# Performance work log

Hardware: AMD Instinct MI355X
Metric: run time of the kernel (lower is better)

The kernel has to match this reference:

```python
import jax, jax.numpy as jnp
import numpy as np

B, P, C = 32, 8732, 21
TOP_K = 200
CONF_THRESH = 0.01
NMS_THRESH = 0.45
VAR0, VAR1 = 0.1, 0.2  # VOC PRIOR_BOX VARIANCE


def setup_inputs() -> dict:
    key = jax.random.key(0)
    k1, k2, k3 = jax.random.split(key, 3)
    loc_data = jax.random.normal(k1, (B, P, 4), jnp.float32)
    conf_data = jax.random.uniform(k2, (B, P, C), jnp.float32)
    prior_data = jax.random.uniform(k3, (P, 4), jnp.float32)
    return {"loc_data": loc_data, "conf_data": conf_data, "prior_data": prior_data}


def _decode(loc, priors):
    # priors are (cx, cy, w, h); returns (x1, y1, x2, y2)
    cxcy = priors[:, :2] + loc[:, :2] * VAR0 * priors[:, 2:]
    wh = priors[:, 2:] * jnp.exp(loc[:, 2:] * VAR1)
    x1y1 = cxcy - wh * 0.5
    return jnp.concatenate([x1y1, x1y1 + wh], axis=1)  # [P,4]


def _nms_class(boxes, scores):
    # boxes [P,4], scores [P] -> [TOP_K,5] rows of (score, x1, y1, x2, y2)
    s = jnp.where(scores > CONF_THRESH, scores, -1.0)
    top_s, idx = jax.lax.top_k(s, TOP_K)          # descending scores
    b = boxes[idx]                                 # [K,4]
    valid = top_s > CONF_THRESH
    x1, y1, x2, y2 = b[:, 0], b[:, 1], b[:, 2], b[:, 3]
    area = (x2 - x1) * (y2 - y1)
    # pairwise intersection / IoU [K,K]
    xx1 = jnp.maximum(x1[:, None], x1[None, :])
    yy1 = jnp.maximum(y1[:, None], y1[None, :])
    xx2 = jnp.minimum(x2[:, None], x2[None, :])
    yy2 = jnp.minimum(y2[:, None], y2[None, :])
    inter = jnp.clip(xx2 - xx1, 0.0) * jnp.clip(yy2 - yy1, 0.0)
    union = area[:, None] + area[None, :] - inter
    iou = inter / union
    ar = jnp.arange(TOP_K)

    def step(carry, j):
        kept, suppressed = carry
        is_kept = valid[j] & ~suppressed[j]
        kept = kept.at[j].set(is_kept)
        suppressed = suppressed | (is_kept & (iou[j] > NMS_THRESH) & (ar > j))
        return (kept, suppressed), None

    (kept, _), _ = jax.lax.scan(
        step, (jnp.zeros(TOP_K, bool), jnp.zeros(TOP_K, bool)), ar)
    # compact kept rows to the front (matches output[i, cl, :count] = ...)
    pos = jnp.cumsum(kept) - 1
    safe = jnp.where(kept, pos, TOP_K)
    rows = jnp.concatenate([top_s[:, None], b], axis=1)  # [K,5]
    out = jnp.zeros((TOP_K + 1, 5), rows.dtype).at[safe].set(rows)[:TOP_K]
    return out


def reference(loc_data, conf_data, prior_data):
    def per_image(loc, conf):
        boxes = _decode(loc, prior_data)           # [P,4]
        return jax.vmap(lambda s: _nms_class(boxes, s), in_axes=1)(conf)  # [C,K,5]

    out = jax.vmap(per_image)(loc_data, conf_data)  # [B,C,K,5]
    return out.at[:, 0].set(0.0)  # class 0 (background) is skipped in original
```

## Files before the change

### kernel.cpp

```cpp
#include <hip/hip_runtime.h>
#include <stdint.h>

#define B_ 32
#define P_ 8732
#define C_ 21
#define TOPK 200
#define TGT 228
#define TGT0 300
#define SUBCAP 28
#define NCH2 35
#define NSLOT (NCH2 * SUBCAP)
#define CONF_T 0.01f
#define NMS_T 0.45f
#define NT 512
#define KV4 5
#define NTASK (B_ * C_)

__device__ __forceinline__ uint32_t f2s(float f) {
    uint32_t u = __float_as_uint(f);
    return (u & 0x80000000u) ? ~u : (u | 0x80000000u);
}
__device__ __forceinline__ float s2f(uint32_t s) {
    uint32_t b = (s & 0x80000000u) ? (s & 0x7FFFFFFFu) : ~s;
    return __uint_as_float(b);
}
__device__ __forceinline__ uint32_t keyof(float v) {
    return f2s((v > CONF_T) ? v : -1.0f);
}
__device__ __forceinline__ uint32_t thr0() {
    return f2s(1.0f - (float)TGT0 / (float)P_);
}

__global__ __launch_bounds__(256) void scatter_cands(const float* __restrict__ conf,
                                                     uint32_t* __restrict__ gccnt,
                                                     uint64_t* __restrict__ gcand) {
    const int b = blockIdx.x / NCH2;
    const int ch = blockIdx.x % NCH2;
    const int p0 = ch * 256;
    const int n = min(256, P_ - p0);
    const int tid = threadIdx.x;
    const int lane = tid & 63;
    const int cs = tid >> 6;
    __shared__ float tile[256 * C_];
    const float4* src4 = (const float4*)(conf + ((size_t)b * P_ + p0) * C_);
    float4* tile4 = (float4*)tile;
    const int tot4 = (n * C_) >> 2;
    for (int i = tid; i < tot4; i += 256) tile4[i] = src4[i];
    __syncthreads();
    const uint32_t T0 = thr0();
    for (int c = (cs == 0 ? 4 : cs); c < C_; c += 4) {
        uint32_t kk[4];
        #pragma unroll
        for (int k = 0; k < 4; ++k) {
            const int r = lane + 64 * k;
            if (r < n) kk[k] = keyof(tile[r * C_ + c]);
            else       kk[k] = 0u;
        }
        const unsigned long long m0 = __ballot(kk[0] >= T0);
        const unsigned long long m1 = __ballot(kk[1] >= T0);
        const unsigned long long m2 = __ballot(kk[2] >= T0);
        const unsigned long long m3 = __ballot(kk[3] >= T0);
        const int c0 = __popcll(m0), c1 = __popcll(m1), c2 = __popcll(m2), c3 = __popcll(m3);
        const int total = c0 + c1 + c2 + c3;
        const int task = b * C_ + c;
        uint64_t* dst = gcand + ((size_t)task * NCH2 + ch) * SUBCAP;
        {
            const unsigned long long below = (1ull << lane) - 1ull;
            const int cum[4] = {0, c0, c0 + c1, c0 + c1 + c2};
            const unsigned long long mm[4] = {m0, m1, m2, m3};
            #pragma unroll
            for (int k = 0; k < 4; ++k) {
                if (kk[k] >= T0) {
                    const int pos = cum[k] + __popcll(mm[k] & below);
                    if (pos < SUBCAP) {
                        const int p = p0 + lane + 64 * k;
                        dst[pos] = ((uint64_t)kk[k] << 32) | (uint32_t)(~(uint32_t)p);
                    }
                }
            }
        }
        if (lane == 0) gccnt[(size_t)task * NCH2 + ch] = (uint32_t)total;
    }
}

template<bool HASWS>
__global__ __launch_bounds__(NT, 6) void detect_kernel(
    const float* __restrict__ loc, const float* __restrict__ prior,
    const uint32_t* __restrict__ gccnt, const uint64_t* __restrict__ gcand,
    const float* __restrict__ conf, float* __restrict__ out)
{
    const int task = blockIdx.x;
    const int b = task / C_;
    const int c = task % C_;
    const int tid = threadIdx.x;
    const int lane = tid & 63;
    float* outp = out + (size_t)task * TOPK * 5;

    if (c == 0) {
        for (int e = tid; e < TOPK * 5; e += NT) outp[e] = 0.0f;
        return;
    }

    __shared__ uint64_t cand[256];
    __shared__ float4 bbox[TOPK];
    __shared__ float bs[TOPK];
    __shared__ float sar[TOPK];
    __shared__ unsigned long long msk[TOPK * 4];
    __shared__ unsigned long long vmask[4];
    __shared__ int order[TOPK];
    __shared__ int s_cnt, s_nk;
    __shared__ int s_c2[2];
    __shared__ int s_c3[3];
    __shared__ uint32_t s_ccnt[NCH2];
    __shared__ int s_gc, s_bad;

    const uint32_t T0 = thr0();

    if (tid == 0) s_cnt = 0;
    if (tid < 2) s_c2[tid] = 0;
    if (tid < 3) s_c3[tid] = 0;
    if (HASWS && tid < NCH2) s_ccnt[tid] = gccnt[(size_t)task * NCH2 + tid];
    for (int i2 = tid; i2 < TOPK * 4; i2 += NT) msk[i2] = 0ull;
    __syncthreads();
    if (HASWS && tid < 64) {
        uint32_t cc = (lane < NCH2) ? s_ccnt[lane] : 0u;
        int bad = (cc > SUBCAP) ? 1 : 0;
        int tot = (int)cc;
        #pragma unroll
        for (int d = 1; d < 64; d <<= 1) {
            tot += __shfl_down(tot, d);
            bad |= __shfl_down(bad, d);
        }
        if (lane == 0) { s_gc = tot; s_bad = bad; }
    }
    __syncthreads();

    const bool fast = HASWS && !s_bad && s_gc >= TOPK;
    const int gc = HASWS ? s_gc : 0;

    uint64_t vc0 = 0, vc1 = 0;
    bool val0 = false, val1 = false;
    uint4 kv[KV4];
    if (fast) {
        const uint64_t* gp = gcand + (size_t)task * NSLOT;
        {
            const int ch0 = tid / SUBCAP, i0 = tid - ch0 * SUBCAP;
            if (i0 < (int)s_ccnt[ch0]) { vc0 = gp[tid]; val0 = true; }
        }
        const int s1 = tid + NT;
        if (s1 < NSLOT) {
            const int ch1 = s1 / SUBCAP, i1 = s1 - ch1 * SUBCAP;
            if (i1 < (int)s_ccnt[ch1]) { vc1 = gp[s1]; val1 = true; }
        }
    } else {
        const float* sp = conf + (size_t)b * P_ * C_ + c;
        #pragma unroll
        for (int r = 0; r < KV4; ++r) {
            uint32_t uu[4];
            #pragma unroll
            for (int c4 = 0; c4 < 4; ++c4) {
                int p = (tid + r * NT) * 4 + c4;
                if (p < P_) {
                    float v = sp[(size_t)p * C_];
                    v = (v > CONF_T) ? v : -1.0f;
                    uu[c4] = f2s(v);
                } else uu[c4] = 0u;
            }
            kv[r] = make_uint4(uu[0], uu[1], uu[2], uu[3]);
        }
    }

    if (fast) {
        const uint32_t k0 = (uint32_t)(vc0 >> 32);
        const uint32_t k1 = (uint32_t)(vc1 >> 32);
        uint32_t vthr = T0;
        if (gc > 256) {
            uint32_t lo = T0, hi = 0xFFFFFFFFu;
            uint32_t t;
            {
                const float sc = s2f(T0);
                const float sn = 1.0f - (1.0f - sc) * (float)TGT / (float)gc;
                t = f2s(sn);
                if (!(t > lo && t < hi)) t = lo + ((hi - lo) >> 1);
            }
            for (int it = 0; ; ++it) {
                const int slot = it % 3;
                int my = (val0 && k0 >= t) + (val1 && k1 >= t);
                #pragma unroll
                for (int d = 1; d < 64; d <<= 1) my += __shfl_down(my, d);
                if (lane == 0) atomicAdd(&s_c3[slot], my);
                if (tid == 0) s_c3[(it + 1) % 3] = 0;
                __syncthreads();
                const int cnt = s_c3[slot];
                if (cnt >= TOPK && cnt <= 256) { vthr = t; break; }
                if (cnt > 256) lo = t; else hi = t;
                if (hi - lo <= 1) { vthr = lo; break; }
                uint32_t tn = 0;
                bool bis = (it >= 8) || (cnt == 0);
                if (!bis) {
                    const float sc = s2f(t);
                    const float sn = 1.0f - (1.0f - sc) * (float)TGT / (float)cnt;
                    tn = f2s(sn);
                    if (!(tn > lo && tn < hi)) bis = true;
                }
                if (bis) tn = lo + ((hi - lo) >> 1);
                t = tn;
            }
        }
        const bool p0v = val0 && k0 >= vthr;
        const bool p1v = val1 && k1 >= vthr;
        const unsigned long long mm0 = __ballot(p0v);
        const unsigned long long mm1 = __ballot(p1v);
        const int wtot = __popcll(mm0) + __popcll(mm1);
        int base = 0;
        if (lane == 0 && wtot) base = atomicAdd(&s_cnt, wtot);
        base = __shfl(base, 0);
        const unsigned long long below = (1ull << lane) - 1ull;
        const int o0 = base + __popcll(mm0 & below);
        const int o1 = base + __popcll(mm0) + __popcll(mm1 & below);
        if (p0v && o0 < 256) cand[o0] = vc0;
        if (p1v && o1 < 256) cand[o1] = vc1;
    } else {
        uint32_t lo = 0u, hi = 0xFFFFFFFFu;
        uint32_t t = f2s(1.0f - (float)TGT / (float)P_);
        uint32_t vthr = 0u;
        for (int it = 0; ; ++it) {
            const int slot = it & 1;
            int my = 0;
            #pragma unroll
            for (int r = 0; r < KV4; ++r)
                my += (kv[r].x >= t) + (kv[r].y >= t) + (kv[r].z >= t) + (kv[r].w >= t);
            #pragma unroll
            for (int d = 1; d < 64; d <<= 1) my += __shfl_down(my, d);
            if (lane == 0) atomicAdd(&s_c2[slot], my);
            __syncthreads();
            const int cnt = s_c2[slot];
            __syncthreads();
            if (tid == 0) s_c2[slot] = 0;
            if (cnt >= TOPK && cnt <= 256) { vthr = t; break; }
            if (cnt > 256) lo = t; else hi = t;
            if (hi - lo <= 1) { vthr = lo; break; }
            uint32_t tn = 0;
            bool bis = (it >= 8) || (cnt == 0);
            if (!bis) {
                const float sc = s2f(t);
                const float sn = 1.0f - (1.0f - sc) * (float)TGT / (float)cnt;
                tn = f2s(sn);
                if (!(tn > lo && tn < hi)) bis = true;
            }
            if (bis) tn = lo + ((hi - lo) >> 1);
            t = tn;
        }
        #pragma unroll
        for (int r = 0; r < KV4; ++r) {
            const int pb = (tid + r * NT) * 4;
            uint32_t uu[4] = {kv[r].x, kv[r].y, kv[r].z, kv[r].w};
            #pragma unroll
            for (int c4 = 0; c4 < 4; ++c4) {
                uint32_t u = uu[c4];
                if (u >= vthr) {
                    int pos = atomicAdd(&s_cnt, 1);
                    if (pos < 256) cand[pos] = ((uint64_t)u << 32) | (uint32_t)(~(uint32_t)(pb + c4));
                }
            }
        }
    }
    __syncthreads();
    if (tid < 256 && tid >= s_cnt) cand[tid] = 0ull;
    __syncthreads();

    uint64_t v = (tid < 256) ? cand[tid] : 0ull;
    for (int kk = 2; kk <= 256; kk <<= 1) {
        for (int j = kk >> 1; j > 0; j >>= 1) {
            if (j >= 64) {
                __syncthreads();
                if (tid < 256) cand[tid] = v;
                __syncthreads();
                if (tid < 256) {
                    uint64_t pv = cand[tid ^ j];
                    bool keepmax = (((tid & j) == 0) == ((tid & kk) == 0));
                    v = keepmax ? (v > pv ? v : pv) : (v < pv ? v : pv);
                }
            } else if (tid < 256) {
                uint64_t pv = __shfl_xor(v, j);
                bool keepmax = (((tid & j) == 0) == ((tid & kk) == 0));
                v = keepmax ? (v > pv ? v : pv) : (v < pv ? v : pv);
            }
        }
    }

    float my_sc = -1.0f;
    if (tid < TOPK) {
        uint32_t su = (uint32_t)(v >> 32);
        int p = (int)(~(uint32_t)v);
        my_sc = s2f(su);
        const float4 l4 = *(const float4*)(loc + ((size_t)b * P_ + p) * 4);
        const float4 pr = *(const float4*)(prior + (size_t)p * 4);
        float cx = __fadd_rn(pr.x, __fmul_rn(__fmul_rn(l4.x, 0.1f), pr.z));
        float cy = __fadd_rn(pr.y, __fmul_rn(__fmul_rn(l4.y, 0.1f), pr.w));
        float ew = (float)exp((double)__fmul_rn(l4.z, 0.2f));
        float eh = (float)exp((double)__fmul_rn(l4.w, 0.2f));
        float w  = __fmul_rn(pr.z, ew);
        float h  = __fmul_rn(pr.w, eh);
        float x1 = __fsub_rn(cx, __fmul_rn(w, 0.5f));
        float y1 = __fsub_rn(cy, __fmul_rn(h, 0.5f));
        float x2 = __fadd_rn(x1, w);
        float y2 = __fadd_rn(y1, h);
        bs[tid] = my_sc;
        bbox[tid] = make_float4(x1, y1, x2, y2);
        sar[tid] = __fmul_rn(__fsub_rn(x2, x1), __fsub_rn(y2, y1));
    }
    {
        unsigned long long bm = __ballot(tid < TOPK && my_sc > CONF_T);
        if (lane == 0 && tid < 256) vmask[tid >> 6] = bm;
    }
    __syncthreads();

    if (tid < 500) {
        const int rp = tid / 5;
        const int s  = tid - rp * 5;
        #pragma unroll
        for (int pass = 0; pass < 2; ++pass) {
            const int j  = pass ? (199 - rp) : rp;
            const int i0 = j + 1 + s;
            const float4 bj = bbox[j];
            const float  aj = sar[j];
            unsigned long long* mrow = &msk[j * 4];
            #pragma unroll
            for (int w = 0; w < 4; ++w) {
                const int wlo = w << 6;
                const int whi = (wlo + 64 < TOPK) ? wlo + 64 : TOPK;
                int i = i0;
                if (i < wlo) i += ((wlo - i + 4) / 5) * 5;
                unsigned long long lw = 0ull;
                for (; i < whi; i += 5) {
                    const float4 bi = bbox[i];
                    float xx1 = fmaxf(bj.x, bi.x);
                    float yy1 = fmaxf(bj.y, bi.y);
                    float xx2 = fminf(bj.z, bi.z);
                    float yy2 = fminf(bj.w, bi.w);
                    float dx = fmaxf(__fsub_rn(xx2, xx1), 0.0f);
                    float dy = fmaxf(__fsub_rn(yy2, yy1), 0.0f);
                    float inter = __fmul_rn(dx, dy);
                    bool sup = false;
                    if (inter > 0.0f) {
                        float ai = sar[i];
                        float uni = __fsub_rn(__fadd_rn(aj, ai), inter);
                        float t45 = __fmul_rn(NMS_T, uni);
                        float mar = __fmul_rn(t45, 1e-6f);
                        sup = inter > __fadd_rn(t45, mar);
                        if (!sup && !(inter < __fsub_rn(t45, mar))) {
                            sup = (inter / uni > NMS_T);
                        }
                    }
                    if (sup) lw |= 1ull << (i & 63);
                }
                if (lw) atomicOr(&mrow[w], lw);
            }
        }
    }
    __syncthreads();

    if (tid < 64) {
        const int L = tid;
        auto or_reduce = [&](unsigned long long x) {
            #pragma unroll
            for (int d = 1; d < 64; d <<= 1) x |= __shfl_xor(x, d);
            return x;
        };
        unsigned long long s1 = 0, s2 = 0, s3 = 0;
        int nk = 0;
        #pragma unroll
        for (int w = 0; w < 4; ++w) {
            const int j = (w << 6) | L;
            unsigned long long r0 = 0, r1 = 0, r2 = 0, r3 = 0;
            if (j < TOPK) {
                const unsigned long long* mr = &msk[j * 4];
                r0 = mr[0]; r1 = mr[1]; r2 = mr[2]; r3 = mr[3];
            }
            const unsigned long long rself = (w == 0) ? r0 : (w == 1) ? r1
                                           : (w == 2) ? r2 : r3;
            unsigned long long sw = (w == 0) ? 0ull : (w == 1) ? s1
                                  : (w == 2) ? s2 : s3;
            unsigned long long alive = vmask[w] & ~sw;
            unsigned long long pm = 0;
            while (alive) {
                int jl = __ffsll(alive) - 1;
                if (L == 0) order[nk] = (w << 6) | jl;
                ++nk;
                sw |= __shfl(rself, jl);
                pm |= (1ull << jl);
                alive &= ~(sw | (1ull << jl));
            }
            if (pm) {
                const bool picked = (pm >> L) & 1ull;
                if (w == 0) {
                    s1 |= or_reduce(picked ? r1 : 0ull);
                    s2 |= or_reduce(picked ? r2 : 0ull);
                    s3 |= or_reduce(picked ? r3 : 0ull);
                } else if (w == 1) {
                    s2 |= or_reduce(picked ? r2 : 0ull);
                    s3 |= or_reduce(picked ? r3 : 0ull);
                } else if (w == 2) {
                    s3 |= or_reduce(picked ? r3 : 0ull);
                }
            }
        }
        if (L == 0) s_nk = nk;
    }
    __syncthreads();

    const int nk = s_nk;
    for (int e = tid; e < TOPK * 5; e += NT) {
        int r = e / 5;
        int f = e - r * 5;
        float val = 0.0f;
        if (r < nk) {
            int j = order[r];
            float4 bb = bbox[j];
            val = (f == 0) ? bs[j] : (f == 1) ? bb.x : (f == 2) ? bb.y
                : (f == 3) ? bb.z : bb.w;
        }
        outp[e] = val;
    }
}

extern "C" void kernel_launch(void* const* d_in, const int* in_sizes, int n_in,
                              void* d_out, int out_size, void* d_ws, size_t ws_size,
                              hipStream_t stream) {
    const float* loc   = (const float*)d_in[0];
    const float* conf  = (const float*)d_in[1];
    const float* prior = (const float*)d_in[2];
    float* out = (float*)d_out;

    const size_t cnt_bytes  = (size_t)NTASK * NCH2 * sizeof(uint32_t);
    const size_t cand_bytes = (size_t)NTASK * NSLOT * sizeof(uint64_t);
    if (ws_size >= cnt_bytes + cand_bytes) {
        uint32_t* gccnt = (uint32_t*)d_ws;
        uint64_t* gcand = (uint64_t*)((char*)d_ws + cnt_bytes);
        scatter_cands<<<B_ * NCH2, 256, 0, stream>>>(conf, gccnt, gcand);
        detect_kernel<true><<<NTASK, NT, 0, stream>>>(loc, prior, gccnt, gcand, conf, out);
    } else {
        detect_kernel<false><<<NTASK, NT, 0, stream>>>(loc, prior, nullptr, nullptr, conf, out);
    }
}
```

Before: 120.9 us.

## Build NMS suppression mask with per-wavefront ballots instead of shared atomics

The pairwise IoU suppression mask is now computed by giving each wavefront one row j per round. Each lane holds four candidate boxes and their areas in registers, and the 64-bit words are formed with __ballot and written directly rather than OR-ed in with shared-memory atomics. Because every word is now written explicitly, the upfront zeroing of the mask array is removed. The intent is to drop atomics, cut LDS reads of bbox[i], and avoid the irregular stride-5 loops, at the cost of idle lanes on the triangular part of the matrix.

```diff
diff --git a/kernel.cpp b/kernel.cpp
--- a/kernel.cpp
+++ b/kernel.cpp
@@ -120,7 +120,6 @@
     if (tid < 2) s_c2[tid] = 0;
     if (tid < 3) s_c3[tid] = 0;
     if (HASWS && tid < NCH2) s_ccnt[tid] = gccnt[(size_t)task * NCH2 + tid];
-    for (int i2 = tid; i2 < TOPK * 4; i2 += NT) msk[i2] = 0ull;
     __syncthreads();
     if (HASWS && tid < 64) {
         uint32_t cc = (lane < NCH2) ? s_ccnt[lane] : 0u;
@@ -316,46 +315,54 @@
     }
     __syncthreads();
 
-    if (tid < 500) {
-        const int rp = tid / 5;
-        const int s  = tid - rp * 5;
-        #pragma unroll
-        for (int pass = 0; pass < 2; ++pass) {
-            const int j  = pass ? (199 - rp) : rp;
-            const int i0 = j + 1 + s;
+    {
+        const int wv = tid >> 6;
+        float4 biA[4];
+        float  aiA[4];
+        #pragma unroll
+        for (int t = 0; t < 4; ++t) {
+            const int i = (t << 6) | lane;
+            if (i < TOPK) {
+                biA[t] = bbox[i];
+                aiA[t] = __fmul_rn(__fsub_rn(biA[t].z, biA[t].x),
+                                   __fsub_rn(biA[t].w, biA[t].y));
+            } else {
+                biA[t] = make_float4(0.0f, 0.0f, 0.0f, 0.0f);
+                aiA[t] = 0.0f;
+            }
+        }
+        for (int r = 0; r < 25; ++r) {
+            const int j = (r << 3) | wv;
             const float4 bj = bbox[j];
             const float  aj = sar[j];
             unsigned long long* mrow = &msk[j * 4];
             #pragma unroll
-            for (int w = 0; w < 4; ++w) {
-                const int wlo = w << 6;
-                const int whi = (wlo + 64 < TOPK) ? wlo + 64 : TOPK;
-                int i = i0;
-                if (i < wlo) i += ((wlo - i + 4) / 5) * 5;
-                unsigned long long lw = 0ull;
-                for (; i < whi; i += 5) {
-                    const float4 bi = bbox[i];
-                    float xx1 = fmaxf(bj.x, bi.x);
-                    float yy1 = fmaxf(bj.y, bi.y);
-                    float xx2 = fminf(bj.z, bi.z);
-                    float yy2 = fminf(bj.w, bi.w);
-                    float dx = fmaxf(__fsub_rn(xx2, xx1), 0.0f);
-                    float dy = fmaxf(__fsub_rn(yy2, yy1), 0.0f);
-                    float inter = __fmul_rn(dx, dy);
+            for (int t = 0; t < 4; ++t) {
+                unsigned long long word = 0ull;
+                if (((t << 6) | 63) > j) {
+                    const int i = (t << 6) | lane;
                     bool sup = false;
-                    if (inter > 0.0f) {
-                        float ai = sar[i];
-                        float uni = __fsub_rn(__fadd_rn(aj, ai), inter);
-                        float t45 = __fmul_rn(NMS_T, uni);
-                        float mar = __fmul_rn(t45, 1e-6f);
-                        sup = inter > __fadd_rn(t45, mar);
-                        if (!sup && !(inter < __fsub_rn(t45, mar))) {
-                            sup = (inter / uni > NMS_T);
+                    if (i > j && i < TOPK) {
+                        const float4 bi = biA[t];
+                        float xx1 = fmaxf(bj.x, bi.x);
+                        float yy1 = fmaxf(bj.y, bi.y);
+                        float xx2 = fminf(bj.z, bi.z);
+                        float yy2 = fminf(bj.w, bi.w);
+                        float dx = fmaxf(__fsub_rn(xx2, xx1), 0.0f);
+                        float dy = fmaxf(__fsub_rn(yy2, yy1), 0.0f);
+                        float inter = __fmul_rn(dx, dy);
+                        if (inter > 0.0f) {
+                            float uni = __fsub_rn(__fadd_rn(aj, aiA[t]), inter);
+                            float t45 = __fmul_rn(NMS_T, uni);
+                            float mar = __fmul_rn(t45, 1e-6f);
+                            sup = inter > __fadd_rn(t45, mar);
+                            if (!sup && !(inter < __fsub_rn(t45, mar)))
+                                sup = (inter / uni > NMS_T);
                         }
                     }
-                    if (sup) lw |= 1ull << (i & 63);
-                }
-                if (lw) atomicOr(&mrow[w], lw);
+                    word = __ballot(sup);
+                }
+                if (lane == 0) mrow[t] = word;
             }
         }
     }
```

Result: slower. 132.2 us (+9.4%).
